# Kernel optimization log

Hardware: AMD Instinct MI355X
Metric: run time of the kernel (lower is better)

## Reference

```python
import jax, jax.numpy as jnp
import numpy as np

HEADS = 8
DIM_HEAD = 64
SCALE = DIM_HEAD ** -0.5


def setup_inputs() -> dict:
    key = jax.random.key(0)
    ks = jax.random.split(key, 7)
    b, p, n, dim = 4, 8, 512, 512
    inner = HEADS * DIM_HEAD
    std = dim ** -0.5
    return {
        "q_in": jax.random.normal(ks[0], (b, p, n, dim), jnp.float32),
        "kv_in": jax.random.normal(ks[1], (b, p, n, dim), jnp.float32),
        "Wq": jax.random.normal(ks[2], (dim, inner), jnp.float32) * std,
        "Wk": jax.random.normal(ks[3], (dim, inner), jnp.float32) * std,
        "Wv": jax.random.normal(ks[4], (dim, inner), jnp.float32) * std,
        "Wo": jax.random.normal(ks[5], (inner, dim), jnp.float32) * std,
        "bo": jnp.zeros((dim,), jnp.float32),
    }


def _split_heads(x):
    # [b, p, n, h*d] -> [b, h, p, n, d]
    b, p, n, hd = x.shape
    return x.reshape(b, p, n, HEADS, DIM_HEAD).transpose(0, 3, 1, 2, 4)


def reference(q_in, kv_in, Wq, Wk, Wv, Wo, bo):
    q = _split_heads(q_in @ Wq)
    k = _split_heads(kv_in @ Wk)
    v = _split_heads(kv_in @ Wv)
    dots = jnp.einsum('bhpid,bhpjd->bhpij', q, k) * SCALE
    attn = jax.nn.softmax(dots, axis=-1)
    out = jnp.einsum('bhpij,bhpjd->bhpid', attn, v)
    # [b, h, p, n, d] -> [b, p, n, h*d]
    b, h, p, n, d = out.shape
    out = out.transpose(0, 2, 3, 1, 4).reshape(b, p, n, h * d)
    return out @ Wo + bo
```

## Files before the change

kernel.cpp:

```cpp
#include <hip/hip_runtime.h>

typedef unsigned short u16;
typedef u16  u16x8 __attribute__((ext_vector_type(8)));
typedef u16  u16x4 __attribute__((ext_vector_type(4)));
typedef float f32x4 __attribute__((ext_vector_type(4)));
typedef __bf16 bf16x8 __attribute__((ext_vector_type(8)));

#define SEQ   512
#define DIM   512
#define DHEAD 64
#define M_ROWS 16384

#define AS1 __attribute__((address_space(1)))
#define AS3 __attribute__((address_space(3)))
#define GLL16(gp, lp) __builtin_amdgcn_global_load_lds((const AS1 void*)(gp), (AS3 void*)(lp), 16, 0, 0)

__device__ __forceinline__ u16 f2b(float f) {
  unsigned int x = __builtin_bit_cast(unsigned int, f);
  return (u16)((x + 0x7fffu + ((x >> 16) & 1u)) >> 16);
}

__global__ __launch_bounds__(256) void convert_in(const float* __restrict__ q,
                                                  const float* __restrict__ kv,
                                                  u16* __restrict__ qb,
                                                  u16* __restrict__ kvb) {
  const float* src = blockIdx.y ? kv : q;
  u16* dst = blockIdx.y ? kvb : qb;
  size_t i = ((size_t)blockIdx.x * 256 + threadIdx.x) * 8;
  float4 a = *reinterpret_cast<const float4*>(&src[i]);
  float4 b = *reinterpret_cast<const float4*>(&src[i + 4]);
  u16x8 o;
  o[0] = f2b(a.x); o[1] = f2b(a.y); o[2] = f2b(a.z); o[3] = f2b(a.w);
  o[4] = f2b(b.x); o[5] = f2b(b.y); o[6] = f2b(b.z); o[7] = f2b(b.w);
  *reinterpret_cast<u16x8*>(&dst[i]) = o;
}

__global__ __launch_bounds__(256) void wtrans(const float* __restrict__ Wq,
                                              const float* __restrict__ Wk,
                                              const float* __restrict__ Wv,
                                              const float* __restrict__ Wo,
                                              u16* __restrict__ out) {
  __shared__ float tile[32][33];
  const int tid = threadIdx.x;
  const int tx = tid & 31, ty = tid >> 5;
  const int z = blockIdx.z;
  const float* W = (z == 0) ? Wq : (z == 1) ? Wk : (z == 2) ? Wv : Wo;
  const int n0 = blockIdx.x * 32;
  const int k0 = blockIdx.y * 32;
#pragma unroll
  for (int i = 0; i < 4; i++) {
    int r = ty + i * 8;
    tile[r][tx] = W[(k0 + r) * DIM + n0 + tx];
  }
  __syncthreads();
  u16* o = out + (size_t)z * DIM * DIM;
#pragma unroll
  for (int i = 0; i < 4; i++) {
    int r = ty + i * 8;
    o[(n0 + r) * DIM + k0 + tx] = f2b(tile[tx][r]);
  }
}

__global__ __launch_bounds__(256) void gemm_qkv(const u16* __restrict__ Qin,
                                                const u16* __restrict__ KVin,
                                                const u16* __restrict__ Wqt,
                                                const u16* __restrict__ Wkt,
                                                const u16* __restrict__ Wvt,
                                                u16* __restrict__ Qb,
                                                u16* __restrict__ Kb,
                                                u16* __restrict__ Vt) {
  __shared__ __attribute__((aligned(16))) u16 As[128 * 32];
  __shared__ __attribute__((aligned(16))) u16 Bs[128 * 32];
  const int tid = threadIdx.x;
  const int lane = tid & 63;
  const int w = tid >> 6;
  const int l15 = lane & 15;
  const int quad = lane >> 4;
  const int z = blockIdx.z;
  const int wr = (w >> 1) * 64, wc = (w & 1) * 64;
  const int srow = lane >> 2;
  const int scol = (lane & 3) * 8;

  int gm, gn;
  const u16 *A, *B;
  if (z < 2) {
    gm = blockIdx.y * 128; gn = blockIdx.x * 128;
    A = z ? KVin : Qin;  B = z ? Wkt : Wqt;
  } else {
    gm = blockIdx.x * 128; gn = blockIdx.y * 128;
    A = Wvt; B = KVin;
  }

  f32x4 acc[4][4] = {};

  for (int k0 = 0; k0 < DIM; k0 += 32) {
    __syncthreads();
#pragma unroll
    for (int i = 0; i < 2; i++) {
      int r0 = w * 32 + i * 16;
      GLL16(&A[(size_t)(gm + r0 + srow) * DIM + k0 + scol], &As[r0 * 32]);
      GLL16(&B[(size_t)(gn + r0 + srow) * DIM + k0 + scol], &Bs[r0 * 32]);
    }
    __syncthreads();

    bf16x8 af[4], bfr[4];
#pragma unroll
    for (int mt = 0; mt < 4; mt++)
      af[mt] = *reinterpret_cast<const bf16x8*>(&As[(wr + mt * 16 + l15) * 32 + quad * 8]);
#pragma unroll
    for (int nt = 0; nt < 4; nt++)
      bfr[nt] = *reinterpret_cast<const bf16x8*>(&Bs[(wc + nt * 16 + l15) * 32 + quad * 8]);
#pragma unroll
    for (int mt = 0; mt < 4; mt++)
#pragma unroll
      for (int nt = 0; nt < 4; nt++)
        acc[mt][nt] = __builtin_amdgcn_mfma_f32_16x16x32_bf16(af[mt], bfr[nt], acc[mt][nt], 0, 0, 0);
  }

  if (z < 2) {
    u16* C = (z == 0) ? Qb : Kb;
#pragma unroll
    for (int mt = 0; mt < 4; mt++)
#pragma unroll
      for (int nt = 0; nt < 4; nt++)
#pragma unroll
        for (int r = 0; r < 4; r++)
          C[(gm + wr + mt * 16 + quad * 4 + r) * DIM + gn + wc + nt * 16 + l15] = f2b(acc[mt][nt][r]);
  } else {
#pragma unroll
    for (int mt = 0; mt < 4; mt++)
#pragma unroll
      for (int nt = 0; nt < 4; nt++)
#pragma unroll
        for (int r = 0; r < 4; r++)
          Vt[(size_t)(gm + wr + mt * 16 + quad * 4 + r) * M_ROWS + gn + wc + nt * 16 + l15] = f2b(acc[mt][nt][r]);
  }
}

__global__ __launch_bounds__(256) void attn(const u16* __restrict__ Qb,
                                            const u16* __restrict__ Kb,
                                            const u16* __restrict__ Vtg,
                                            u16* __restrict__ Ob) {
  __shared__ u16 Qs[64 * 72];
  __shared__ u16 Ks[64 * 72];
  __shared__ u16 Vs[64 * 72];
  __shared__ u16 Pq[4][16 * 72];

  const int tid = threadIdx.x;
  const int lane = tid & 63;
  const int w = tid >> 6;
  const int l15 = lane & 15;
  const int quad = lane >> 4;

  const int bid = blockIdx.x;
  const int qt = bid & 7;
  const int bhp = bid >> 3;
  const int h = bhp & 7;
  const int bp = bhp >> 3;
  const int qrow0 = bp * SEQ + qt * 64;
  const int col0 = h * DHEAD;

#pragma unroll
  for (int i = 0; i < 2; i++) {
    int idx = tid + i * 256;
    int row = idx >> 3, c = idx & 7;
    u16x8 v = *reinterpret_cast<const u16x8*>(&Qb[(qrow0 + row) * DIM + col0 + c * 8]);
    *reinterpret_cast<u16x8*>(&Qs[row * 72 + c * 8]) = v;
  }
  __syncthreads();

  bf16x8 qf[2];
#pragma unroll
  for (int kd = 0; kd < 2; kd++)
    qf[kd] = *reinterpret_cast<const bf16x8*>(&Qs[(w * 16 + l15) * 72 + kd * 32 + quad * 8]);

  float m_ = -1e30f, l_ = 0.0f;
  f32x4 o[4] = {};

  for (int j = 0; j < 8; j++) {
    __syncthreads();
#pragma unroll
    for (int i = 0; i < 2; i++) {
      int idx = tid + i * 256;
      int row = idx >> 3, c = idx & 7;
      u16x8 v = *reinterpret_cast<const u16x8*>(&Kb[(bp * SEQ + j * 64 + row) * DIM + col0 + c * 8]);
      *reinterpret_cast<u16x8*>(&Ks[row * 72 + c * 8]) = v;
    }
#pragma unroll
    for (int i = 0; i < 2; i++) {
      int idx = tid + i * 256;
      int row = idx >> 3, c = idx & 7;
      u16x8 v = *reinterpret_cast<const u16x8*>(&Vtg[(size_t)(col0 + row) * M_ROWS + bp * SEQ + j * 64 + c * 8]);
      *reinterpret_cast<u16x8*>(&Vs[row * 72 + c * 8]) = v;
    }
    __syncthreads();

    f32x4 st[4];
#pragma unroll
    for (int ct = 0; ct < 4; ct++) {
      f32x4 zacc = {};
#pragma unroll
      for (int kd = 0; kd < 2; kd++) {
        bf16x8 kf = *reinterpret_cast<const bf16x8*>(&Ks[(ct * 16 + l15) * 72 + kd * 32 + quad * 8]);
        zacc = __builtin_amdgcn_mfma_f32_16x16x32_bf16(kf, qf[kd], zacc, 0, 0, 0);
      }
      st[ct] = zacc * 0.125f;
    }

    float pm = -1e30f;
#pragma unroll
    for (int ct = 0; ct < 4; ct++)
#pragma unroll
      for (int r = 0; r < 4; r++) pm = fmaxf(pm, st[ct][r]);
    pm = fmaxf(pm, __shfl_xor(pm, 16));
    pm = fmaxf(pm, __shfl_xor(pm, 32));
    float mn = fmaxf(m_, pm);
    float alpha = __expf(m_ - mn);
    m_ = mn;
    float rs = 0.0f;
#pragma unroll
    for (int ct = 0; ct < 4; ct++)
#pragma unroll
      for (int r = 0; r < 4; r++) {
        float pv = __expf(st[ct][r] - mn);
        st[ct][r] = pv;
        rs += pv;
      }
    rs += __shfl_xor(rs, 16);
    rs += __shfl_xor(rs, 32);
    l_ = l_ * alpha + rs;
#pragma unroll
    for (int r = 0; r < 4; r++) {
      float ar = __shfl(alpha, quad * 4 + r);
#pragma unroll
      for (int nt = 0; nt < 4; nt++) o[nt][r] *= ar;
    }

#pragma unroll
    for (int t = 0; t < 4; t++) {
      u16x4 pk;
#pragma unroll
      for (int e = 0; e < 4; e++) pk[e] = f2b(st[t][e]);
      *reinterpret_cast<u16x4*>(&Pq[w][l15 * 72 + t * 16 + quad * 4]) = pk;
    }
    __threadfence_block();

#pragma unroll
    for (int c = 0; c < 2; c++) {
      bf16x8 af = *reinterpret_cast<const bf16x8*>(&Pq[w][l15 * 72 + c * 32 + quad * 8]);
#pragma unroll
      for (int nt = 0; nt < 4; nt++) {
        bf16x8 bv = *reinterpret_cast<const bf16x8*>(&Vs[(nt * 16 + l15) * 72 + c * 32 + quad * 8]);
        o[nt] = __builtin_amdgcn_mfma_f32_16x16x32_bf16(af, bv, o[nt], 0, 0, 0);
      }
    }
  }

  float inv = 1.0f / l_;
#pragma unroll
  for (int r = 0; r < 4; r++) {
    float lr = __shfl(inv, quad * 4 + r);
#pragma unroll
    for (int nt = 0; nt < 4; nt++)
      Ob[(qrow0 + w * 16 + quad * 4 + r) * DIM + col0 + nt * 16 + l15] = f2b(o[nt][r] * lr);
  }
}

__global__ __launch_bounds__(256) void gemm_out(const u16* __restrict__ Ab,
                                                const u16* __restrict__ Bt,
                                                const float* __restrict__ bias,
                                                float* __restrict__ C) {
  __shared__ __attribute__((aligned(16))) u16 As[128 * 32];
  __shared__ __attribute__((aligned(16))) u16 Bs[128 * 32];
  const int tid = threadIdx.x;
  const int lane = tid & 63;
  const int w = tid >> 6;
  const int l15 = lane & 15;
  const int quad = lane >> 4;
  const int gm = blockIdx.y * 128;
  const int gn = blockIdx.x * 128;
  const int wr = (w >> 1) * 64, wc = (w & 1) * 64;
  const int srow = lane >> 2;
  const int scol = (lane & 3) * 8;

  f32x4 acc[4][4] = {};

  for (int k0 = 0; k0 < DIM; k0 += 32) {
    __syncthreads();
#pragma unroll
    for (int i = 0; i < 2; i++) {
      int r0 = w * 32 + i * 16;
      GLL16(&Ab[(size_t)(gm + r0 + srow) * DIM + k0 + scol], &As[r0 * 32]);
      GLL16(&Bt[(size_t)(gn + r0 + srow) * DIM + k0 + scol], &Bs[r0 * 32]);
    }
    __syncthreads();

    bf16x8 af[4], bfr[4];
#pragma unroll
    for (int mt = 0; mt < 4; mt++)
      af[mt] = *reinterpret_cast<const bf16x8*>(&As[(wr + mt * 16 + l15) * 32 + quad * 8]);
#pragma unroll
    for (int nt = 0; nt < 4; nt++)
      bfr[nt] = *reinterpret_cast<const bf16x8*>(&Bs[(wc + nt * 16 + l15) * 32 + quad * 8]);
#pragma unroll
    for (int mt = 0; mt < 4; mt++)
#pragma unroll
      for (int nt = 0; nt < 4; nt++)
        acc[mt][nt] = __builtin_amdgcn_mfma_f32_16x16x32_bf16(af[mt], bfr[nt], acc[mt][nt], 0, 0, 0);
  }

#pragma unroll
  for (int mt = 0; mt < 4; mt++)
#pragma unroll
    for (int nt = 0; nt < 4; nt++) {
      float bcol = bias[gn + wc + nt * 16 + l15];
#pragma unroll
      for (int r = 0; r < 4; r++)
        C[(gm + wr + mt * 16 + quad * 4 + r) * DIM + gn + wc + nt * 16 + l15] = acc[mt][nt][r] + bcol;
    }
}

extern "C" void kernel_launch(void* const* d_in, const int* in_sizes, int n_in,
                              void* d_out, int out_size, void* d_ws, size_t ws_size,
                              hipStream_t stream) {
  const float* q_in  = (const float*)d_in[0];
  const float* kv_in = (const float*)d_in[1];
  const float* Wq    = (const float*)d_in[2];
  const float* Wk    = (const float*)d_in[3];
  const float* Wv    = (const float*)d_in[4];
  const float* Wo    = (const float*)d_in[5];
  const float* bo    = (const float*)d_in[6];
  float* out = (float*)d_out;

  u16* ws = (u16*)d_ws;
  u16* Wqt = ws;
  u16* Wkt = ws + 262144;
  u16* Wvt = ws + 524288;
  u16* Wot = ws + 786432;
  u16* Qb  = ws + 1048576;
  u16* Kb  = Qb + (size_t)M_ROWS * DIM;
  u16* Vtg = Kb + (size_t)M_ROWS * DIM;
  u16* Ob  = Vtg + (size_t)M_ROWS * DIM;
  u16* Qin_b  = (u16*)d_out;
  u16* KVin_b = Qin_b + (size_t)M_ROWS * DIM;

  convert_in<<<dim3(4096, 2), 256, 0, stream>>>(q_in, kv_in, Qin_b, KVin_b);
  wtrans<<<dim3(16, 16, 4), 256, 0, stream>>>(Wq, Wk, Wv, Wo, ws);
  gemm_qkv<<<dim3(4, 128, 3), 256, 0, stream>>>(Qin_b, KVin_b, Wqt, Wkt, Wvt, Qb, Kb, Vtg);
  attn<<<dim3(2048), 256, 0, stream>>>(Qb, Kb, Vtg, Ob);
  gemm_out<<<dim3(4, 128), 256, 0, stream>>>(Ob, Wot, bo, out);
}
```

Measured before the change: 237.8 us.

## Enlarge attention tiles to 128 queries and keys, load K/V via global_load_lds

The attention kernel now processes 128 query rows per block (two 16-row groups per wave) and 128-key chunks per iteration, halving the grid and the number of K/V reloads per query. K and V tiles are loaded directly into LDS with global_load_lds in an unpadded plane layout, and Q fragments are read straight from global memory instead of staging through LDS. The aim is more reuse of each loaded K/V tile and fewer loop iterations and barriers, at the cost of more registers, fewer blocks, and possible LDS bank conflicts from the unpadded layout.

```diff
diff --git a/kernel.cpp b/kernel.cpp
--- a/kernel.cpp
+++ b/kernel.cpp
@@ -141,128 +141,132 @@
                                             const u16* __restrict__ Kb,
                                             const u16* __restrict__ Vtg,
                                             u16* __restrict__ Ob) {
-  __shared__ u16 Qs[64 * 72];
-  __shared__ u16 Ks[64 * 72];
-  __shared__ u16 Vs[64 * 72];
-  __shared__ u16 Pq[4][16 * 72];
+  __shared__ __attribute__((aligned(16))) u16 Ks[2 * 128 * 32];
+  __shared__ __attribute__((aligned(16))) u16 Vs[4 * 64 * 32];
+  __shared__ __attribute__((aligned(16))) u16 Pq[4][16 * 136];
 
   const int tid = threadIdx.x;
   const int lane = tid & 63;
   const int w = tid >> 6;
   const int l15 = lane & 15;
   const int quad = lane >> 4;
+  const int srow = lane >> 2;
+  const int scol = (lane & 3) * 8;
 
   const int bid = blockIdx.x;
-  const int qt = bid & 7;
-  const int bhp = bid >> 3;
+  const int qt = bid & 3;
+  const int bhp = bid >> 2;
   const int h = bhp & 7;
   const int bp = bhp >> 3;
-  const int qrow0 = bp * SEQ + qt * 64;
+  const int qrow0 = bp * SEQ + qt * 128;
   const int col0 = h * DHEAD;
 
-#pragma unroll
-  for (int i = 0; i < 2; i++) {
-    int idx = tid + i * 256;
-    int row = idx >> 3, c = idx & 7;
-    u16x8 v = *reinterpret_cast<const u16x8*>(&Qb[(qrow0 + row) * DIM + col0 + c * 8]);
-    *reinterpret_cast<u16x8*>(&Qs[row * 72 + c * 8]) = v;
-  }
-  __syncthreads();
-
-  bf16x8 qf[2];
-#pragma unroll
-  for (int kd = 0; kd < 2; kd++)
-    qf[kd] = *reinterpret_cast<const bf16x8*>(&Qs[(w * 16 + l15) * 72 + kd * 32 + quad * 8]);
-
-  float m_ = -1e30f, l_ = 0.0f;
-  f32x4 o[4] = {};
-
-  for (int j = 0; j < 8; j++) {
-    __syncthreads();
-#pragma unroll
-    for (int i = 0; i < 2; i++) {
-      int idx = tid + i * 256;
-      int row = idx >> 3, c = idx & 7;
-      u16x8 v = *reinterpret_cast<const u16x8*>(&Kb[(bp * SEQ + j * 64 + row) * DIM + col0 + c * 8]);
-      *reinterpret_cast<u16x8*>(&Ks[row * 72 + c * 8]) = v;
-    }
-#pragma unroll
-    for (int i = 0; i < 2; i++) {
-      int idx = tid + i * 256;
-      int row = idx >> 3, c = idx & 7;
-      u16x8 v = *reinterpret_cast<const u16x8*>(&Vtg[(size_t)(col0 + row) * M_ROWS + bp * SEQ + j * 64 + c * 8]);
-      *reinterpret_cast<u16x8*>(&Vs[row * 72 + c * 8]) = v;
-    }
-    __syncthreads();
-
-    f32x4 st[4];
-#pragma unroll
-    for (int ct = 0; ct < 4; ct++) {
-      f32x4 zacc = {};
-#pragma unroll
-      for (int kd = 0; kd < 2; kd++) {
-        bf16x8 kf = *reinterpret_cast<const bf16x8*>(&Ks[(ct * 16 + l15) * 72 + kd * 32 + quad * 8]);
-        zacc = __builtin_amdgcn_mfma_f32_16x16x32_bf16(kf, qf[kd], zacc, 0, 0, 0);
+  bf16x8 qf[2][2];
+#pragma unroll
+  for (int g = 0; g < 2; g++)
+#pragma unroll
+    for (int kd = 0; kd < 2; kd++)
+      qf[g][kd] = *reinterpret_cast<const bf16x8*>(
+          &Qb[(size_t)(qrow0 + w * 32 + g * 16 + l15) * DIM + col0 + kd * 32 + quad * 8]);
+
+  float m_[2] = {-1e30f, -1e30f}, l_[2] = {0.0f, 0.0f};
+  f32x4 o[2][4] = {};
+
+  for (int j = 0; j < 4; j++) {
+    __syncthreads();
+    const int krow0 = bp * SEQ + j * 128;
+#pragma unroll
+    for (int i = 0; i < 4; i++) {
+      int t = w * 4 + i;
+      int plane = t & 1, chunk = t >> 1;
+      GLL16(&Kb[(size_t)(krow0 + chunk * 16 + srow) * DIM + col0 + plane * 32 + scol],
+            &Ks[plane * 4096 + chunk * 512]);
+    }
+#pragma unroll
+    for (int i = 0; i < 4; i++) {
+      int t = w * 4 + i;
+      int plane = t & 3, chunk = t >> 2;
+      GLL16(&Vtg[(size_t)(col0 + chunk * 16 + srow) * M_ROWS + krow0 + plane * 32 + scol],
+            &Vs[plane * 2048 + chunk * 512]);
+    }
+    __syncthreads();
+
+#pragma unroll
+    for (int g = 0; g < 2; g++) {
+      f32x4 st[8];
+#pragma unroll
+      for (int ct = 0; ct < 8; ct++) {
+        f32x4 z = {};
+#pragma unroll
+        for (int kd = 0; kd < 2; kd++) {
+          bf16x8 kf = *reinterpret_cast<const bf16x8*>(&Ks[kd * 4096 + (ct * 16 + l15) * 32 + quad * 8]);
+          z = __builtin_amdgcn_mfma_f32_16x16x32_bf16(kf, qf[g][kd], z, 0, 0, 0);
+        }
+        st[ct] = z * 0.125f;
       }
-      st[ct] = zacc * 0.125f;
-    }
-
-    float pm = -1e30f;
-#pragma unroll
-    for (int ct = 0; ct < 4; ct++)
-#pragma unroll
-      for (int r = 0; r < 4; r++) pm = fmaxf(pm, st[ct][r]);
-    pm = fmaxf(pm, __shfl_xor(pm, 16));
-    pm = fmaxf(pm, __shfl_xor(pm, 32));
-    float mn = fmaxf(m_, pm);
-    float alpha = __expf(m_ - mn);
-    m_ = mn;
-    float rs = 0.0f;
-#pragma unroll
-    for (int ct = 0; ct < 4; ct++)
+
+      float pm = -1e30f;
+#pragma unroll
+      for (int ct = 0; ct < 8; ct++)
+#pragma unroll
+        for (int r = 0; r < 4; r++) pm = fmaxf(pm, st[ct][r]);
+      pm = fmaxf(pm, __shfl_xor(pm, 16));
+      pm = fmaxf(pm, __shfl_xor(pm, 32));
+      float mn = fmaxf(m_[g], pm);
+      float alpha = __expf(m_[g] - mn);
+      m_[g] = mn;
+      float rs = 0.0f;
+#pragma unroll
+      for (int ct = 0; ct < 8; ct++)
+#pragma unroll
+        for (int r = 0; r < 4; r++) {
+          float pv = __expf(st[ct][r] - mn);
+          st[ct][r] = pv;
+          rs += pv;
+        }
+      rs += __shfl_xor(rs, 16);
+      rs += __shfl_xor(rs, 32);
+      l_[g] = l_[g] * alpha + rs;
 #pragma unroll
       for (int r = 0; r < 4; r++) {
-        float pv = __expf(st[ct][r] - mn);
-        st[ct][r] = pv;
-        rs += pv;
+        float ar = __shfl(alpha, quad * 4 + r);
+#pragma unroll
+        for (int nt = 0; nt < 4; nt++) o[g][nt][r] *= ar;
       }
-    rs += __shfl_xor(rs, 16);
-    rs += __shfl_xor(rs, 32);
-    l_ = l_ * alpha + rs;
+
+#pragma unroll
+      for (int ct = 0; ct < 8; ct++) {
+        u16x4 pk;
+#pragma unroll
+        for (int e = 0; e < 4; e++) pk[e] = f2b(st[ct][e]);
+        *reinterpret_cast<u16x4*>(&Pq[w][l15 * 136 + ct * 16 + quad * 4]) = pk;
+      }
+      __threadfence_block();
+
+#pragma unroll
+      for (int c2 = 0; c2 < 4; c2++) {
+        bf16x8 af = *reinterpret_cast<const bf16x8*>(&Pq[w][l15 * 136 + c2 * 32 + quad * 8]);
+#pragma unroll
+        for (int nt = 0; nt < 4; nt++) {
+          bf16x8 bv = *reinterpret_cast<const bf16x8*>(&Vs[c2 * 2048 + (nt * 16 + l15) * 32 + quad * 8]);
+          o[g][nt] = __builtin_amdgcn_mfma_f32_16x16x32_bf16(af, bv, o[g][nt], 0, 0, 0);
+        }
+      }
+      __threadfence_block();
+    }
+  }
+
+#pragma unroll
+  for (int g = 0; g < 2; g++) {
+    float inv = 1.0f / l_[g];
 #pragma unroll
     for (int r = 0; r < 4; r++) {
-      float ar = __shfl(alpha, quad * 4 + r);
-#pragma unroll
-      for (int nt = 0; nt < 4; nt++) o[nt][r] *= ar;
-    }
-
-#pragma unroll
-    for (int t = 0; t < 4; t++) {
-      u16x4 pk;
-#pragma unroll
-      for (int e = 0; e < 4; e++) pk[e] = f2b(st[t][e]);
-      *reinterpret_cast<u16x4*>(&Pq[w][l15 * 72 + t * 16 + quad * 4]) = pk;
-    }
-    __threadfence_block();
-
-#pragma unroll
-    for (int c = 0; c < 2; c++) {
-      bf16x8 af = *reinterpret_cast<const bf16x8*>(&Pq[w][l15 * 72 + c * 32 + quad * 8]);
-#pragma unroll
-      for (int nt = 0; nt < 4; nt++) {
-        bf16x8 bv = *reinterpret_cast<const bf16x8*>(&Vs[(nt * 16 + l15) * 72 + c * 32 + quad * 8]);
-        o[nt] = __builtin_amdgcn_mfma_f32_16x16x32_bf16(af, bv, o[nt], 0, 0, 0);
-      }
-    }
-  }
-
-  float inv = 1.0f / l_;
-#pragma unroll
-  for (int r = 0; r < 4; r++) {
-    float lr = __shfl(inv, quad * 4 + r);
-#pragma unroll
-    for (int nt = 0; nt < 4; nt++)
-      Ob[(qrow0 + w * 16 + quad * 4 + r) * DIM + col0 + nt * 16 + l15] = f2b(o[nt][r] * lr);
+      float lr = __shfl(inv, quad * 4 + r);
+      int row = qrow0 + w * 32 + g * 16 + quad * 4 + r;
+#pragma unroll
+      for (int nt = 0; nt < 4; nt++)
+        Ob[(size_t)row * DIM + col0 + nt * 16 + l15] = f2b(o[g][nt][r] * lr);
+    }
   }
 }
 
@@ -347,6 +351,6 @@
   convert_in<<<dim3(4096, 2), 256, 0, stream>>>(q_in, kv_in, Qin_b, KVin_b);
   wtrans<<<dim3(16, 16, 4), 256, 0, stream>>>(Wq, Wk, Wv, Wo, ws);
   gemm_qkv<<<dim3(4, 128, 3), 256, 0, stream>>>(Qin_b, KVin_b, Wqt, Wkt, Wvt, Qb, Kb, Vtg);
-  attn<<<dim3(2048), 256, 0, stream>>>(Qb, Kb, Vtg, Ob);
+  attn<<<dim3(1024), 256, 0, stream>>>(Qb, Kb, Vtg, Ob);
   gemm_out<<<dim3(4, 128), 256, 0, stream>>>(Ob, Wot, bo, out);
 }
```

After: 233.5 us. About the same (-1.8%).
